# Kernel optimization log

Measured on AMD Instinct MI355X. Metric: run time of the kernel, lower is better.

## Reference

```python
import jax, jax.numpy as jnp
import numpy as np

ON_OFF = "off"  # init kwarg: 'off' includes the next-frame temporal candidate

def setup_inputs() -> dict:
    key = jax.random.key(0)
    k1, k2 = jax.random.split(key)
    xs = jax.random.normal(k1, (4, 32, 128, 32), dtype=jnp.float32)  # [B,T,N,D]
    A = jax.random.randint(k2, (1, 128, 128), 0, 2, dtype=jnp.int32)  # [1,N,N] adjacency
    return {"xs": xs, "A": A}

def reference(xs, A):
    B, T, N, D = xs.shape
    # A_f = A + I ; neighbors are nonzero entries (self-loop included via eye)
    A_f = A[0].astype(xs.dtype) + jnp.eye(N, dtype=xs.dtype)
    spatial_mask = A_f != 0  # [N,N] : spatial_mask[n, j] -> j is neighbor of n

    # Candidate set per (frame t, node n): prev-frame self, next-frame self (on_off=='off'),
    # and all spatial neighbors at frame t. Padded to fixed size K = N + 2 with masks.
    spat = jnp.broadcast_to(xs[:, :, None, :, :], (B, T, N, N, D))   # [B,T,N,N,D]
    prev = jnp.concatenate([xs[:, :1], xs[:, :-1]], axis=1)          # [B,T,N,D] (t=0 masked)
    nxt = jnp.concatenate([xs[:, 1:], xs[:, -1:]], axis=1)           # [B,T,N,D] (t=T-1 masked)
    cand = jnp.concatenate([prev[:, :, :, None, :], nxt[:, :, :, None, :], spat], axis=3)  # [B,T,N,N+2,D]

    t = jnp.arange(T)
    prev_m = jnp.broadcast_to((t > 0)[:, None, None], (T, N, 1))
    if ON_OFF == "off":
        next_m = jnp.broadcast_to((t < T - 1)[:, None, None], (T, N, 1))
    else:
        next_m = jnp.zeros((T, N, 1), dtype=bool)
    sp_m = jnp.broadcast_to(spatial_mask[None], (T, N, N))
    mask = jnp.concatenate([prev_m, next_m, sp_m], axis=2)  # [T,N,N+2]

    # Masked median = torch.median semantics (lower median): sort with +inf padding,
    # pick index (k-1)//2 where k = number of valid candidates.
    vals = jnp.where(mask[None, :, :, :, None], cand, jnp.inf)
    vals = jnp.sort(vals, axis=3)
    k = mask.sum(axis=2)              # [T,N]
    med_idx = (k - 1) // 2            # lower median index
    idx = jnp.broadcast_to(med_idx[None, :, :, None, None], (B, T, N, 1, D))
    ys = jnp.take_along_axis(vals, idx, axis=3)[:, :, :, 0, :]  # [B,T,N,D]
    return ys
```

## Files before the change

kernel.cpp:

```cpp
#include <hip/hip_runtime.h>
#include <stdint.h>
#include <math.h>

#define BB 4
#define TT 32
#define NN 128
#define DD 32
#define NPB 8
#define NBLK (BB * TT * (NN / NPB))
#define CAP 16

__device__ __forceinline__ int bin8(float x) {
    int i = (int)fmaf(x, 5.0f, 4.0f);
    i = i < 0 ? 0 : i;
    return i > 7 ? 7 : i;
}

__global__ __launch_bounds__(64) void build_adj_kernel(const int* __restrict__ A,
                                                       int* __restrict__ deg,
                                                       uint8_t* __restrict__ nbr) {
    const int n = blockIdx.x;
    const int lane = threadIdx.x;
    const int* arow = A + n * NN;
    uint8_t* row = nbr + n * NN;
    const int j0 = lane, j1 = lane + 64;
    const bool b0 = (arow[j0] != 0) || (j0 == n);
    const bool b1 = (arow[j1] != 0) || (j1 == n);
    const unsigned long long m0 = __ballot(b0);
    const unsigned long long m1 = __ballot(b1);
    const unsigned long long lmask = (1ULL << lane) - 1ULL;
    const int c0 = __popcll(m0);
    if (b0) row[__popcll(m0 & lmask)] = (uint8_t)j0;
    if (b1) row[c0 + __popcll(m1 & lmask)] = (uint8_t)j1;
    if (lane == 0) deg[n] = c0 + __popcll(m1);
}

__global__ __launch_bounds__(256) void median_kernel(const float* __restrict__ xs,
                                                     const int* __restrict__ deg,
                                                     const uint8_t* __restrict__ nbr,
                                                     float* __restrict__ out) {
    __shared__ float sval[NN * DD];
    __shared__ uint32_t snbr_w[NPB * NN / 4];
    __shared__ int sdeg[NPB];
    __shared__ float slist[(CAP + 1) * 256];

    const int tid = threadIdx.x;
    const int g = blockIdx.x;
    const int ng = g % (NN / NPB);
    const int t  = (g / (NN / NPB)) % TT;
    const int b  = g / ((NN / NPB) * TT);
    const int n0 = ng * NPB;

    const int d = tid & (DD - 1);
    const int nl = tid >> 5;
    const int n = n0 + nl;
    const int pv = (t > 0) ? 1 : 0;
    const int nv = (t < TT - 1) ? 1 : 0;
    const int ne = pv + nv;

    float exv0 = 0.0f, exv1 = 0.0f;
    if (pv) exv0 = xs[(((size_t)(b * TT + t - 1) * NN) + n) * DD + d];
    if (nv) {
        float v = xs[(((size_t)(b * TT + t + 1) * NN) + n) * DD + d];
        if (pv) exv1 = v; else exv0 = v;
    }

    const float4* src4 = (const float4*)(xs + ((size_t)(b * TT + t) * NN) * DD);
    #pragma unroll
    for (int s = 0; s < 4; ++s) {
        int i4 = tid + (s << 8);
        ((float4*)sval)[i4] = src4[i4];
    }
    snbr_w[tid] = ((const uint32_t*)(nbr + (size_t)n0 * NN))[tid];
    if (tid < NPB) sdeg[tid] = deg[n0 + tid];
    __syncthreads();

    const int dg = sdeg[nl];
    const int k = dg + ne;
    const uint32_t r = (uint32_t)((k - 1) >> 1);
    const uint8_t* nb = (const uint8_t*)snbr_w + nl * NN;
    const float INFV = __uint_as_float(0x7F800000u);

    unsigned long long pcnt = 0ull;
    {
        int j = 0;
        for (; j + 4 <= dg; j += 4) {
            uint32_t nw = *(const uint32_t*)(nb + j);
            #pragma unroll
            for (int q = 0; q < 4; ++q) {
                float x = sval[((nw >> (q * 8)) & 0xFFu) * DD + d];
                pcnt += 1ull << (bin8(x) * 8);
            }
        }
        for (; j < dg; ++j) {
            float x = sval[nb[j] * DD + d];
            pcnt += 1ull << (bin8(x) * 8);
        }
        if (ne >= 1) pcnt += 1ull << (bin8(exv0) * 8);
        if (ne == 2) pcnt += 1ull << (bin8(exv1) * 8);
    }

    uint32_t cum = 0, lowcnt = 0, mexp = 0;
    int selbin = -1;
    #pragma unroll
    for (int bb = 0; bb < 8; ++bb) {
        uint32_t bc = (uint32_t)(pcnt >> (bb * 8)) & 0xFFu;
        uint32_t nc = cum + bc;
        if (selbin < 0 && r < nc) { selbin = bb; lowcnt = cum; mexp = bc; }
        cum = nc;
    }
    const bool fb = (mexp > CAP);
    const uint32_t rp = r - lowcnt;
    const int storebin = fb ? -1 : selbin;

    int mc = 0;
    {
        int j = 0;
        for (; j + 4 <= dg; j += 4) {
            uint32_t nw = *(const uint32_t*)(nb + j);
            #pragma unroll
            for (int q = 0; q < 4; ++q) {
                float x = sval[((nw >> (q * 8)) & 0xFFu) * DD + d];
                int slot = mc > CAP ? CAP : mc;
                slist[slot * 256 + tid] = x;
                mc += (bin8(x) == storebin);
            }
        }
        for (; j < dg; ++j) {
            float x = sval[nb[j] * DD + d];
            int slot = mc > CAP ? CAP : mc;
            slist[slot * 256 + tid] = x;
            mc += (bin8(x) == storebin);
        }
        if (ne >= 1) {
            int slot = mc > CAP ? CAP : mc;
            slist[slot * 256 + tid] = exv0;
            mc += (bin8(exv0) == storebin);
        }
        if (ne == 2) {
            int slot = mc > CAP ? CAP : mc;
            slist[slot * 256 + tid] = exv1;
            mc += (bin8(exv1) == storebin);
        }
    }

    float ki[CAP];
    uint32_t cn[CAP];
    #pragma unroll
    for (int u = 0; u < CAP; ++u) {
        float v = slist[u * 256 + tid];
        ki[u] = (u < mc) ? v : INFV;
        cn[u] = 0;
    }
    int mm = mc;
    #pragma unroll
    for (int off = 32; off; off >>= 1) {
        int o = __shfl_xor(mm, off);
        mm = mm > o ? mm : o;
    }
    for (int j = 0; j < mm; ++j) {
        float x = slist[j * 256 + tid];
        x = (j < mc) ? x : INFV;
        #pragma unroll
        for (int u = 0; u < CAP; ++u) cn[u] += (x < ki[u]);
    }
    float result = 0.0f;
    bool found = fb;
    #pragma unroll
    for (int u = 0; u < CAP; ++u) {
        if (!found && u < mc && cn[u] == rp) { result = ki[u]; found = true; }
    }

    if (__ballot(!found)) {
        uint32_t eq[CAP];
        #pragma unroll
        for (int u = 0; u < CAP; ++u) eq[u] = 0;
        for (int j = 0; j < mm; ++j) {
            float x = slist[j * 256 + tid];
            x = (j < mc) ? x : INFV;
            #pragma unroll
            for (int u = 0; u < CAP; ++u) eq[u] += (x == ki[u]);
        }
        #pragma unroll
        for (int u = 0; u < CAP; ++u) {
            if (!found && u < mc && cn[u] <= rp && rp < cn[u] + eq[u]) {
                result = ki[u]; found = true;
            }
        }
    }

    if (__ballot(fb)) {
        bool done = !fb;
        for (int i0 = 0; __ballot(!done && i0 < k); i0 += 8) {
            float k8[8]; uint32_t c8[8];
            #pragma unroll
            for (int u = 0; u < 8; ++u) {
                int i = i0 + u;
                float sv = sval[nb[i & 127] * DD + d];
                float ev = ((i - dg) == 0) ? exv0 : exv1;
                float v = (i < dg) ? sv : ev;
                k8[u] = (i < k) ? v : INFV;
                c8[u] = 0;
            }
            for (int j = 0; j < dg; ++j) {
                float xv = sval[nb[j] * DD + d];
                #pragma unroll
                for (int u = 0; u < 8; ++u) c8[u] += (xv < k8[u]);
            }
            if (ne >= 1) {
                #pragma unroll
                for (int u = 0; u < 8; ++u) c8[u] += (exv0 < k8[u]);
            }
            if (ne == 2) {
                #pragma unroll
                for (int u = 0; u < 8; ++u) c8[u] += (exv1 < k8[u]);
            }
            #pragma unroll
            for (int u = 0; u < 8; ++u) {
                if (!done && (i0 + u) < k && c8[u] == r) { result = k8[u]; done = true; }
            }
        }
        if (__ballot(!done)) {
            for (int i0 = 0; __ballot(!done && i0 < k); i0 += 4) {
                float k4[4]; uint32_t lt4[4], le4[4];
                #pragma unroll
                for (int u = 0; u < 4; ++u) {
                    int i = i0 + u;
                    float sv = sval[nb[i & 127] * DD + d];
                    float ev = ((i - dg) == 0) ? exv0 : exv1;
                    float v = (i < dg) ? sv : ev;
                    k4[u] = (i < k) ? v : INFV;
                    lt4[u] = 0; le4[u] = 0;
                }
                for (int j = 0; j < dg; ++j) {
                    float xv = sval[nb[j] * DD + d];
                    #pragma unroll
                    for (int u = 0; u < 4; ++u) { lt4[u] += (xv < k4[u]); le4[u] += (xv <= k4[u]); }
                }
                if (ne >= 1) {
                    #pragma unroll
                    for (int u = 0; u < 4; ++u) { lt4[u] += (exv0 < k4[u]); le4[u] += (exv0 <= k4[u]); }
                }
                if (ne == 2) {
                    #pragma unroll
                    for (int u = 0; u < 4; ++u) { lt4[u] += (exv1 < k4[u]); le4[u] += (exv1 <= k4[u]); }
                }
                #pragma unroll
                for (int u = 0; u < 4; ++u) {
                    if (!done && (i0 + u) < k && lt4[u] <= r && r < le4[u]) {
                        result = k4[u]; done = true;
                    }
                }
            }
        }
    }

    out[(((size_t)(b * TT + t) * NN) + n) * DD + d] = result;
}

extern "C" void kernel_launch(void* const* d_in, const int* in_sizes, int n_in,
                              void* d_out, int out_size, void* d_ws, size_t ws_size,
                              hipStream_t stream) {
    const float* xs = (const float*)d_in[0];
    const int* A = (const int*)d_in[1];
    float* out = (float*)d_out;

    int* deg = (int*)d_ws;
    uint8_t* nbr = (uint8_t*)d_ws + 512;

    build_adj_kernel<<<NN, 64, 0, stream>>>(A, deg, nbr);
    median_kernel<<<NBLK, 256, 0, stream>>>(xs, deg, nbr, out);
}
```

Measured before the change: 123.4 us.

## Store candidate indices instead of values, double nodes per block, swizzle block order

The per-thread band list now holds 16-bit candidate indices in shared memory rather than float values, and values are re-read from the shared frame tile (or the prev/next registers) when needed. This halves the slist footprint, which makes room for 16 nodes per 512-thread block so each staged frame tile serves twice as many nodes. Block indices are also permuted so neighbouring blocks map to different (b,t) groups. The cost is an extra indirect shared load and two selects per band access, plus a larger block.

```diff
diff --git a/kernel.cpp b/kernel.cpp
--- a/kernel.cpp
+++ b/kernel.cpp
@@ -6,9 +6,13 @@
 #define TT 32
 #define NN 128
 #define DD 32
-#define NPB 8
+#define NPB 16
+#define TPB (NPB * DD)
 #define NBLK (BB * TT * (NN / NPB))
 #define CAP 16
+
+#define SID_PREV 0xFFFEu
+#define SID_NEXT 0xFFFFu
 
 __device__ __forceinline__ int bin8(float x) {
     int i = (int)fmaf(x, 5.0f, 4.0f);
@@ -35,20 +39,21 @@
     if (lane == 0) deg[n] = c0 + __popcll(m1);
 }
 
-__global__ __launch_bounds__(256) void median_kernel(const float* __restrict__ xs,
+__global__ __launch_bounds__(TPB) void median_kernel(const float* __restrict__ xs,
                                                      const int* __restrict__ deg,
                                                      const uint8_t* __restrict__ nbr,
                                                      float* __restrict__ out) {
     __shared__ float sval[NN * DD];
     __shared__ uint32_t snbr_w[NPB * NN / 4];
     __shared__ int sdeg[NPB];
-    __shared__ float slist[(CAP + 1) * 256];
+    __shared__ uint16_t slist[(CAP + 1) * TPB];
 
     const int tid = threadIdx.x;
-    const int g = blockIdx.x;
-    const int ng = g % (NN / NPB);
-    const int t  = (g / (NN / NPB)) % TT;
-    const int b  = g / ((NN / NPB) * TT);
+    const int bid = blockIdx.x;
+    const int g = ((bid & 7) << 7) | (bid >> 3);
+    const int ng = g & (NN / NPB - 1);
+    const int t  = (g >> 3) & (TT - 1);
+    const int b  = g >> 8;
     const int n0 = ng * NPB;
 
     const int d = tid & (DD - 1);
@@ -67,8 +72,8 @@
 
     const float4* src4 = (const float4*)(xs + ((size_t)(b * TT + t) * NN) * DD);
     #pragma unroll
-    for (int s = 0; s < 4; ++s) {
-        int i4 = tid + (s << 8);
+    for (int s = 0; s < 2; ++s) {
+        int i4 = tid + (s << 9);
         ((float4*)sval)[i4] = src4[i4];
     }
     snbr_w[tid] = ((const uint32_t*)(nbr + (size_t)n0 * NN))[tid];
@@ -120,35 +125,45 @@
             uint32_t nw = *(const uint32_t*)(nb + j);
             #pragma unroll
             for (int q = 0; q < 4; ++q) {
-                float x = sval[((nw >> (q * 8)) & 0xFFu) * DD + d];
+                uint32_t id = (nw >> (q * 8)) & 0xFFu;
+                float x = sval[id * DD + d];
                 int slot = mc > CAP ? CAP : mc;
-                slist[slot * 256 + tid] = x;
+                slist[slot * TPB + tid] = (uint16_t)id;
                 mc += (bin8(x) == storebin);
             }
         }
         for (; j < dg; ++j) {
-            float x = sval[nb[j] * DD + d];
+            uint32_t id = nb[j];
+            float x = sval[id * DD + d];
             int slot = mc > CAP ? CAP : mc;
-            slist[slot * 256 + tid] = x;
+            slist[slot * TPB + tid] = (uint16_t)id;
             mc += (bin8(x) == storebin);
         }
         if (ne >= 1) {
             int slot = mc > CAP ? CAP : mc;
-            slist[slot * 256 + tid] = exv0;
+            slist[slot * TPB + tid] = (uint16_t)SID_PREV;
             mc += (bin8(exv0) == storebin);
         }
         if (ne == 2) {
             int slot = mc > CAP ? CAP : mc;
-            slist[slot * 256 + tid] = exv1;
+            slist[slot * TPB + tid] = (uint16_t)SID_NEXT;
             mc += (bin8(exv1) == storebin);
         }
     }
+
+    auto bandval = [&](int e) -> float {
+        uint32_t id = slist[e * TPB + tid];
+        float v = sval[(id & 127u) * DD + d];
+        v = (id == SID_PREV) ? exv0 : v;
+        v = (id == SID_NEXT) ? exv1 : v;
+        return v;
+    };
 
     float ki[CAP];
     uint32_t cn[CAP];
     #pragma unroll
     for (int u = 0; u < CAP; ++u) {
-        float v = slist[u * 256 + tid];
+        float v = bandval(u);
         ki[u] = (u < mc) ? v : INFV;
         cn[u] = 0;
     }
@@ -159,7 +174,7 @@
         mm = mm > o ? mm : o;
     }
     for (int j = 0; j < mm; ++j) {
-        float x = slist[j * 256 + tid];
+        float x = bandval(j);
         x = (j < mc) ? x : INFV;
         #pragma unroll
         for (int u = 0; u < CAP; ++u) cn[u] += (x < ki[u]);
@@ -176,7 +191,7 @@
         #pragma unroll
         for (int u = 0; u < CAP; ++u) eq[u] = 0;
         for (int j = 0; j < mm; ++j) {
-            float x = slist[j * 256 + tid];
+            float x = bandval(j);
             x = (j < mc) ? x : INFV;
             #pragma unroll
             for (int u = 0; u < CAP; ++u) eq[u] += (x == ki[u]);
@@ -269,5 +284,5 @@
     uint8_t* nbr = (uint8_t*)d_ws + 512;
 
     build_adj_kernel<<<NN, 64, 0, stream>>>(A, deg, nbr);
-    median_kernel<<<NBLK, 256, 0, stream>>>(xs, deg, nbr, out);
-}
+    median_kernel<<<NBLK, TPB, 0, stream>>>(xs, deg, nbr, out);
+}
```

After: 128.0 us. 3.7% more time.
